# Optimization experiments

Hardware: AMD Instinct MI355X
Metric: run time of the kernel (lower is better)

The kernel has to match this reference:

```python
import jax, jax.numpy as jnp
import numpy as np

T, N, E = 512, 64, 1024   # encoder frames, batch, encoder feature dim
H = 320                   # pred_hidden_size
J = 512                   # joint hidden
V = 29                    # vocab incl. blank
BLANK = V - 1
MAX_SYM = 30              # max_symbols_per_step


def setup_inputs() -> dict:
    key = jax.random.key(0)
    ks = jax.random.split(key, 16)
    sH = 1.0 / np.sqrt(H)
    sE = 1.0 / np.sqrt(E)
    sJ = 1.0 / np.sqrt(J)
    b_o = jax.random.normal(ks[14], (V,), jnp.float32) * 0.1
    b_o = b_o.at[BLANK].add(4.0)  # blank-dominant logits -> realistic sparse emissions
    return {
        "f": jax.random.normal(ks[0], (T, N, E), jnp.float32),
        "f_lens": jax.random.randint(ks[1], (N,), T // 2, T + 1).astype(jnp.int32),
        "emb": jax.random.normal(ks[2], (V - 1, H), jnp.float32) * 0.1,
        "wi0": jax.random.normal(ks[3], (4 * H, H), jnp.float32) * sH,
        "wh0": jax.random.normal(ks[4], (4 * H, H), jnp.float32) * sH,
        "bi0": jax.random.normal(ks[5], (4 * H,), jnp.float32) * 0.05,
        "bh0": jax.random.normal(ks[6], (4 * H,), jnp.float32) * 0.05,
        "wi1": jax.random.normal(ks[7], (4 * H, H), jnp.float32) * sH,
        "wh1": jax.random.normal(ks[8], (4 * H, H), jnp.float32) * sH,
        "bi1": jax.random.normal(ks[9], (4 * H,), jnp.float32) * 0.05,
        "bh1": jax.random.normal(ks[10], (4 * H,), jnp.float32) * 0.05,
        "w_f": jax.random.normal(ks[11], (J, E), jnp.float32) * sE,
        "w_g": jax.random.normal(ks[12], (J, H), jnp.float32) * sH,
        "b_j": jax.random.normal(ks[13], (J,), jnp.float32) * 0.05,
        "w_o": jax.random.normal(ks[15], (V, J), jnp.float32) * sJ,
        "b_o": b_o,
    }


def reference(f, f_lens, emb, wi0, wh0, bi0, bh0, wi1, wh1, bi1, bh1,
              w_f, w_g, b_j, w_o, b_o):
    n = f.shape[1]
    rows = jnp.arange(n)

    def cell(x, h, c, wi, wh, bi, bh):
        g = x @ wi.T + h @ wh.T + (bi + bh)
        i, fg, gg, o = jnp.split(g, 4, axis=-1)  # torch LSTM gate order i,f,g,o
        c2 = jax.nn.sigmoid(fg) * c + jax.nn.sigmoid(i) * jnp.tanh(gg)
        return jax.nn.sigmoid(o) * jnp.tanh(c2), c2

    def pred_step(last_sym, h, c):
        # SOS (=-1) embeds to zeros
        x = jnp.where(last_sym[:, None] < 0, 0.0, emb[jnp.clip(last_sym, 0, V - 2)])
        h0, c0 = cell(x, h[0], c[0], wi0, wh0, bi0, bh0)
        h1, c1 = cell(h0, h[1], c[1], wi1, wh1, bi1, bh1)
        return h1, jnp.stack([h0, h1]), jnp.stack([c0, c1])

    def joint(fi, g):
        hj = jax.nn.relu(fi @ w_f.T + g @ w_g.T + b_j)
        return hj @ w_o.T + b_o

    def cond(st):
        return jnp.any(st[0] < f_lens)

    def body(st):
        time_idx, sym_add, res, res_idx, last, h, c = st
        fi = f[jnp.clip(time_idx, 0, T - 1), rows]            # [N,E] per-element frame
        g, h_new, c_new = pred_step(last, h, c)               # one LSTM step
        sym = jnp.argmax(joint(fi, g), axis=1).astype(jnp.int32)
        active = time_idx < f_lens
        emit = active & (sym != BLANK) & (sym_add < MAX_SYM)
        adv = active & ~emit                                   # blank or symbol cap -> advance time
        slot = jnp.where(emit, res_idx + 1, 0)
        res = res.at[rows, slot].set(jnp.where(emit, sym, res[rows, slot]))
        res_idx = res_idx + emit.astype(jnp.int32)
        sym_add = jnp.where(emit, sym_add + 1, jnp.where(adv, 0, sym_add))
        time_idx = time_idx + adv.astype(jnp.int32)
        last = jnp.where(emit, sym, last)
        m = emit[None, :, None]
        return (time_idx, sym_add, res, res_idx, last,
                jnp.where(m, h_new, h), jnp.where(m, c_new, c))

    init = (jnp.zeros((n,), jnp.int32),                        # time_idx
            jnp.zeros((n,), jnp.int32),                        # symbols_added
            jnp.full((n, MAX_SYM * T), -1, jnp.int32),         # res
            jnp.full((n,), -1, jnp.int32),                     # res_idx
            jnp.full((n,), -1, jnp.int32),                     # pred_g (SOS)
            jnp.zeros((2, n, H), jnp.float32),                 # pred h
            jnp.zeros((2, n, H), jnp.float32))                 # pred c
    st = jax.lax.while_loop(cond, body, init)
    res, res_idx = st[2], st[3]
    return res, res_idx + 1
```

## Files before the change

### kernel.cpp

```cpp
#include <hip/hip_runtime.h>
#include <math.h>

#define T_ 512
#define N_ 64
#define E_ 1024
#define H_ 320
#define HS8_ 40
#define J_ 512
#define V_ 29
#define BLANK_ 28
#define MAXSYM_ 30
#define RESW_ (MAXSYM_ * T_)

__device__ float g_Xi0[V_][4 * H_];
__device__ float g_b1s[4 * H_];
__device__ float g_h0x[2][N_][H_];
__device__ float g_h1x[2][N_][H_];
__device__ float g_gpx[2][N_][8][J_];
__device__ unsigned int g_flag[N_];

#define BM_ 128
#define BN_ 128
#define BK_ 16

__global__ __launch_bounds__(256) void fproj_gemm(
    const float* __restrict__ A, const float* __restrict__ B,
    const float* __restrict__ bj, float* __restrict__ C) {
  __shared__ __align__(16) float As[BK_][BM_ + 4];
  __shared__ __align__(16) float Bs[BK_][BN_ + 4];
  const int tid = threadIdx.x;
  const int m0 = blockIdx.x * BM_;
  const int j0 = blockIdx.y * BN_;
  const int tx = tid & 15, ty = tid >> 4;
  const int sm = tid >> 1;
  const int sk = (tid & 1) << 3;

  float acc[8][8];
#pragma unroll
  for (int i = 0; i < 8; ++i)
#pragma unroll
    for (int j = 0; j < 8; ++j) acc[i][j] = 0.f;

  for (int kc = 0; kc < E_; kc += BK_) {
    float4 av0 = *(const float4*)(A + (size_t)(m0 + sm) * E_ + kc + sk);
    float4 av1 = *(const float4*)(A + (size_t)(m0 + sm) * E_ + kc + sk + 4);
    float4 bv0 = *(const float4*)(B + (size_t)(j0 + sm) * E_ + kc + sk);
    float4 bv1 = *(const float4*)(B + (size_t)(j0 + sm) * E_ + kc + sk + 4);
    __syncthreads();
    As[sk + 0][sm] = av0.x; As[sk + 1][sm] = av0.y;
    As[sk + 2][sm] = av0.z; As[sk + 3][sm] = av0.w;
    As[sk + 4][sm] = av1.x; As[sk + 5][sm] = av1.y;
    As[sk + 6][sm] = av1.z; As[sk + 7][sm] = av1.w;
    Bs[sk + 0][sm] = bv0.x; Bs[sk + 1][sm] = bv0.y;
    Bs[sk + 2][sm] = bv0.z; Bs[sk + 3][sm] = bv0.w;
    Bs[sk + 4][sm] = bv1.x; Bs[sk + 5][sm] = bv1.y;
    Bs[sk + 6][sm] = bv1.z; Bs[sk + 7][sm] = bv1.w;
    __syncthreads();
#pragma unroll
    for (int k = 0; k < BK_; ++k) {
      float a_[8], b_[8];
      *(float4*)&a_[0] = *(const float4*)&As[k][ty * 8];
      *(float4*)&a_[4] = *(const float4*)&As[k][ty * 8 + 4];
      *(float4*)&b_[0] = *(const float4*)&Bs[k][tx * 8];
      *(float4*)&b_[4] = *(const float4*)&Bs[k][tx * 8 + 4];
#pragma unroll
      for (int i = 0; i < 8; ++i)
#pragma unroll
        for (int j = 0; j < 8; ++j) acc[i][j] += a_[i] * b_[j];
    }
  }

#pragma unroll
  for (int i = 0; i < 8; ++i) {
    const size_t m = (size_t)(m0 + ty * 8 + i);
#pragma unroll
    for (int j = 0; j < 8; j += 4) {
      float4 v;
      v.x = acc[i][j + 0] + bj[j0 + tx * 8 + j + 0];
      v.y = acc[i][j + 1] + bj[j0 + tx * 8 + j + 1];
      v.z = acc[i][j + 2] + bj[j0 + tx * 8 + j + 2];
      v.w = acc[i][j + 3] + bj[j0 + tx * 8 + j + 3];
      *(float4*)(C + m * J_ + j0 + tx * 8 + j) = v;
    }
  }
}

__global__ void init_kernel(int* __restrict__ res) {
  const int idx = blockIdx.x * blockDim.x + threadIdx.x;
  if (idx < N_) g_flag[idx] = 0u;
  const int stride = gridDim.x * blockDim.x;
  for (size_t i = idx; i < (size_t)N_ * RESW_; i += stride) res[i] = -1;
}

__global__ __launch_bounds__(256) void xi0_kernel(
    const float* __restrict__ emb, const float* __restrict__ wi0,
    const float* __restrict__ bi0, const float* __restrict__ bh0,
    const float* __restrict__ bi1, const float* __restrict__ bh1) {
  __shared__ __align__(16) float xs[H_];
  const int s = blockIdx.x;
  const int tid = threadIdx.x;
  for (int i = tid; i < H_; i += 256)
    xs[i] = (s < V_ - 1) ? emb[(size_t)s * H_ + i] : 0.f;
  __syncthreads();
  for (int o = tid; o < 4 * H_; o += 256) {
    float acc = bi0[o] + bh0[o];
    if (s < V_ - 1) {
      const float* wr = wi0 + (size_t)o * H_;
      for (int k = 0; k < H_; k += 4) {
        float4 x4 = *(const float4*)&xs[k];
        float4 w4 = *(const float4*)&wr[k];
        acc += x4.x * w4.x + x4.y * w4.y + x4.z * w4.z + x4.w * w4.w;
      }
    }
    g_Xi0[s][o] = acc;
    if (s == 0) g_b1s[o] = bi1[o] + bh1[o];
  }
}

__device__ __forceinline__ float sigmoidf_(float x) {
  return 1.f / (1.f + expf(-x));
}

__device__ __forceinline__ void flag_round8(int row, int tid, int& target) {
  target += 8;
  __syncthreads();
  if (tid == 0) {
    __hip_atomic_fetch_add(&g_flag[row], 1u, __ATOMIC_RELEASE,
                           __HIP_MEMORY_SCOPE_AGENT);
    while (__hip_atomic_load(&g_flag[row], __ATOMIC_ACQUIRE,
                             __HIP_MEMORY_SCOPE_AGENT) < (unsigned)target)
      __builtin_amdgcn_s_sleep(2);
  }
  __syncthreads();
}

__device__ void recompute8(
    int s, int row, int k8, int tid, int par, int& target,
    const float* __restrict__ wh0, const float* __restrict__ wi1,
    const float* __restrict__ wh1, const float* __restrict__ w_g,
    float* h0s, float* h1s, float* gates,
    float& c0, float& c1, float2& gp) {
  const int g = tid / HS8_;
  const int il = tid - g * HS8_;
  const int o = g * H_ + k8 * HS8_ + il;

  if (tid < 4 * HS8_) {
    const float* wr = wh0 + (size_t)o * H_;
    float acc = g_Xi0[s][o];
    for (int kk = 0; kk < H_; kk += 4) {
      float4 h4 = *(const float4*)&h0s[kk];
      float4 w4 = *(const float4*)&wr[kk];
      acc += h4.x * w4.x + h4.y * w4.y + h4.z * w4.z + h4.w * w4.w;
    }
    gates[tid] = acc;
  }
  __syncthreads();
  if (tid < HS8_) {
    float ig = sigmoidf_(gates[tid]);
    float fg = sigmoidf_(gates[HS8_ + tid]);
    float gg = tanhf(gates[2 * HS8_ + tid]);
    float og = sigmoidf_(gates[3 * HS8_ + tid]);
    float c2 = fg * c0 + ig * gg;
    c0 = c2;
    float h2 = og * tanhf(c2);
    __hip_atomic_store(&g_h0x[par][row][k8 * HS8_ + tid], h2, __ATOMIC_RELAXED,
                       __HIP_MEMORY_SCOPE_AGENT);
  }
  float acc1 = 0.f;
  if (tid < 4 * HS8_) {
    const float* whr = wh1 + (size_t)o * H_;
    acc1 = g_b1s[o];
    for (int kk = 0; kk < H_; kk += 4) {
      float4 h4 = *(const float4*)&h1s[kk];
      float4 w4 = *(const float4*)&whr[kk];
      acc1 += h4.x * w4.x + h4.y * w4.y + h4.z * w4.z + h4.w * w4.w;
    }
  }
  flag_round8(row, tid, target);
  h0s[tid] = __hip_atomic_load(&g_h0x[par][row][tid], __ATOMIC_RELAXED,
                               __HIP_MEMORY_SCOPE_AGENT);
  if (tid < H_ - 256)
    h0s[256 + tid] = __hip_atomic_load(&g_h0x[par][row][256 + tid],
                                       __ATOMIC_RELAXED, __HIP_MEMORY_SCOPE_AGENT);
  __syncthreads();
  if (tid < 4 * HS8_) {
    const float* wir = wi1 + (size_t)o * H_;
    for (int kk = 0; kk < H_; kk += 4) {
      float4 x4 = *(const float4*)&h0s[kk];
      float4 w4 = *(const float4*)&wir[kk];
      acc1 += x4.x * w4.x + x4.y * w4.y + x4.z * w4.z + x4.w * w4.w;
    }
    gates[tid] = acc1;
  }
  __syncthreads();
  if (tid < HS8_) {
    float ig = sigmoidf_(gates[tid]);
    float fg = sigmoidf_(gates[HS8_ + tid]);
    float gg = tanhf(gates[2 * HS8_ + tid]);
    float og = sigmoidf_(gates[3 * HS8_ + tid]);
    float c2 = fg * c1 + ig * gg;
    c1 = c2;
    float h2 = og * tanhf(c2);
    h1s[k8 * HS8_ + tid] = h2;
    __hip_atomic_store(&g_h1x[par][row][k8 * HS8_ + tid], h2, __ATOMIC_RELAXED,
                       __HIP_MEMORY_SCOPE_AGENT);
  }
  __syncthreads();
  {
    const float* hsl = &h1s[k8 * HS8_];
#pragma unroll
    for (int jj = 0; jj < 2; ++jj) {
      const int j = tid + jj * 256;
      const float* wgr = w_g + (size_t)j * H_ + k8 * HS8_;
      float a = 0.f;
      for (int kk = 0; kk < HS8_; kk += 4) {
        float4 h4 = *(const float4*)&hsl[kk];
        float4 w4 = *(const float4*)&wgr[kk];
        a += h4.x * w4.x + h4.y * w4.y + h4.z * w4.z + h4.w * w4.w;
      }
      __hip_atomic_store(&g_gpx[par][row][k8][j], a, __ATOMIC_RELAXED,
                         __HIP_MEMORY_SCOPE_AGENT);
    }
  }
  flag_round8(row, tid, target);
  {
    float ax = 0.f, ay = 0.f;
#pragma unroll
    for (int kk = 0; kk < 8; ++kk) {
      ax += __hip_atomic_load(&g_gpx[par][row][kk][2 * tid], __ATOMIC_RELAXED,
                              __HIP_MEMORY_SCOPE_AGENT);
      ay += __hip_atomic_load(&g_gpx[par][row][kk][2 * tid + 1], __ATOMIC_RELAXED,
                              __HIP_MEMORY_SCOPE_AGENT);
    }
    gp.x = ax; gp.y = ay;
  }
  h1s[tid] = __hip_atomic_load(&g_h1x[par][row][tid], __ATOMIC_RELAXED,
                               __HIP_MEMORY_SCOPE_AGENT);
  if (tid < H_ - 256)
    h1s[256 + tid] = __hip_atomic_load(&g_h1x[par][row][256 + tid],
                                       __ATOMIC_RELAXED, __HIP_MEMORY_SCOPE_AGENT);
  __syncthreads();
}

__global__ __launch_bounds__(256, 2) void decode8(
    const float* __restrict__ Fproj, const int* __restrict__ f_lens,
    const float* __restrict__ wh0,
    const float* __restrict__ wi1, const float* __restrict__ wh1,
    const float* __restrict__ w_g,
    const float* __restrict__ w_o, const float* __restrict__ b_o,
    int* __restrict__ res, int* __restrict__ nsym) {
  const int bid = blockIdx.x;
  const int k8 = bid & 7;
  const int row = ((bid >> 3) + 8 * k8) & 63;
  const int tid = threadIdx.x;
  const int f_len = f_lens[row];

  __shared__ __align__(16) float h0s[H_], h1s[H_];
  __shared__ __align__(16) float gates[4 * HS8_];
  __shared__ __align__(16) float hjs[J_];
  __shared__ float logits[32];

  const int v = tid >> 3;
  const int lq = tid & 7;
  float4 wo[16];
  float bo = 0.f;
  if (v < V_) {
#pragma unroll
    for (int q = 0; q < 16; ++q)
      wo[q] = *(const float4*)(w_o + (size_t)v * J_ + lq * 4 + 32 * q);
    bo = b_o[v];
  }

  for (int i = tid; i < H_; i += 256) { h0s[i] = 0.f; h1s[i] = 0.f; }
  float c0 = 0.f, c1 = 0.f;
  float2 gp = {0.f, 0.f};
  int target = 0;
  __syncthreads();

  recompute8(BLANK_, row, k8, tid, 0, target, wh0, wi1, wh1, w_g,
             h0s, h1s, gates, c0, c1, gp);
  int ecount = 1;

  int t_loc = 0, sym_add = 0, res_idx = -1;
  float2 fp = *(const float2*)(Fproj + (size_t)row * J_ + 2 * tid);

  while (t_loc < f_len) {
    const int tn = (t_loc + 1 < T_) ? t_loc + 1 : T_ - 1;
    float2 fpn = *(const float2*)(Fproj + ((size_t)tn * N_ + row) * J_ + 2 * tid);

    float hx = fp.x + gp.x, hy = fp.y + gp.y;
    float2 hj2 = {hx > 0.f ? hx : 0.f, hy > 0.f ? hy : 0.f};
    *(float2*)&hjs[2 * tid] = hj2;
    __syncthreads();

    float p = 0.f;
    if (v < V_) {
#pragma unroll
      for (int q = 0; q < 16; ++q) {
        float4 h4 = *(const float4*)&hjs[lq * 4 + 32 * q];
        p += h4.x * wo[q].x + h4.y * wo[q].y + h4.z * wo[q].z + h4.w * wo[q].w;
      }
    }
    p += __shfl_xor(p, 4, 8);
    p += __shfl_xor(p, 2, 8);
    p += __shfl_xor(p, 1, 8);
    if (v < V_ && lq == 0) logits[v] = p + bo;
    __syncthreads();

    float best = logits[0];
    int bi = 0;
#pragma unroll
    for (int vv = 1; vv < V_; ++vv) {
      float lv = logits[vv];
      if (lv > best) { best = lv; bi = vv; }
    }
    const int emit = (bi != BLANK_) && (sym_add < MAXSYM_);

    if (emit) {
      res_idx += 1;
      if (k8 == 0 && tid == 0) res[(size_t)row * RESW_ + res_idx] = bi;
      sym_add += 1;
      recompute8(bi, row, k8, tid, ecount & 1, target, wh0, wi1, wh1, w_g,
                 h0s, h1s, gates, c0, c1, gp);
      ecount += 1;
    } else {
      sym_add = 0;
      t_loc += 1;
      fp = fpn;
    }
  }

  if (k8 == 0 && tid == 0) nsym[row] = res_idx + 1;
}

extern "C" void kernel_launch(void* const* d_in, const int* in_sizes, int n_in,
                              void* d_out, int out_size, void* d_ws, size_t ws_size,
                              hipStream_t stream) {
  const float* f      = (const float*)d_in[0];
  const int*   f_lens = (const int*)d_in[1];
  const float* emb    = (const float*)d_in[2];
  const float* wi0    = (const float*)d_in[3];
  const float* wh0    = (const float*)d_in[4];
  const float* bi0    = (const float*)d_in[5];
  const float* bh0    = (const float*)d_in[6];
  const float* wi1    = (const float*)d_in[7];
  const float* wh1    = (const float*)d_in[8];
  const float* bi1    = (const float*)d_in[9];
  const float* bh1    = (const float*)d_in[10];
  const float* w_f    = (const float*)d_in[11];
  const float* w_g    = (const float*)d_in[12];
  const float* b_j    = (const float*)d_in[13];
  const float* w_o    = (const float*)d_in[14];
  const float* b_o    = (const float*)d_in[15];

  int* out  = (int*)d_out;
  int* res  = out;
  int* nsym = out + (size_t)N_ * RESW_;

  float* Fproj = (float*)d_ws;

  init_kernel<<<1024, 256, 0, stream>>>(res);
  xi0_kernel<<<V_, 256, 0, stream>>>(emb, wi0, bi0, bh0, bi1, bh1);

  dim3 ggrid(T_ * N_ / BM_, J_ / BN_);
  fproj_gemm<<<ggrid, 256, 0, stream>>>(f, w_f, b_j, Fproj);

  decode8<<<N_ * 8, 256, 0, stream>>>(Fproj, f_lens, wh0, wi1, wh1, w_g,
                                      w_o, b_o, res, nsym);
}
```

Measured before the change: 1.996 ms.

## Fuse encoder projection GEMM into decode kernel with per-tile readiness flags

Merges the Fproj GEMM and the greedy decode into one launch. The first 512 blocks run the decoder and the remaining 1024 blocks compute GEMM tiles, each tile bumping a g_done counter for its pair of timesteps. Decoder blocks spin on those counters before reading the next frame's projection, so decoding overlaps with the GEMM instead of waiting for it to finish. It also folds the xi0 precompute into the init kernel and shortens the spin sleep. The scheme relies on all decoder blocks being co-resident with the GEMM blocks (launch bounds of 4 blocks per CU) to avoid deadlock, and GEMM blocks now compete with decoding for CU resources.

```diff
diff --git a/kernel.cpp b/kernel.cpp
--- a/kernel.cpp
+++ b/kernel.cpp
@@ -12,108 +12,51 @@
 #define MAXSYM_ 30
 #define RESW_ (MAXSYM_ * T_)
 
+#define BM_ 128
+#define BN_ 128
+#define BK_ 16
+#define DECB_ 512
+
 __device__ float g_Xi0[V_][4 * H_];
 __device__ float g_b1s[4 * H_];
 __device__ float g_h0x[2][N_][H_];
 __device__ float g_h1x[2][N_][H_];
 __device__ float g_gpx[2][N_][8][J_];
 __device__ unsigned int g_flag[N_];
-
-#define BM_ 128
-#define BN_ 128
-#define BK_ 16
-
-__global__ __launch_bounds__(256) void fproj_gemm(
-    const float* __restrict__ A, const float* __restrict__ B,
-    const float* __restrict__ bj, float* __restrict__ C) {
-  __shared__ __align__(16) float As[BK_][BM_ + 4];
-  __shared__ __align__(16) float Bs[BK_][BN_ + 4];
-  const int tid = threadIdx.x;
-  const int m0 = blockIdx.x * BM_;
-  const int j0 = blockIdx.y * BN_;
-  const int tx = tid & 15, ty = tid >> 4;
-  const int sm = tid >> 1;
-  const int sk = (tid & 1) << 3;
-
-  float acc[8][8];
-#pragma unroll
-  for (int i = 0; i < 8; ++i)
-#pragma unroll
-    for (int j = 0; j < 8; ++j) acc[i][j] = 0.f;
-
-  for (int kc = 0; kc < E_; kc += BK_) {
-    float4 av0 = *(const float4*)(A + (size_t)(m0 + sm) * E_ + kc + sk);
-    float4 av1 = *(const float4*)(A + (size_t)(m0 + sm) * E_ + kc + sk + 4);
-    float4 bv0 = *(const float4*)(B + (size_t)(j0 + sm) * E_ + kc + sk);
-    float4 bv1 = *(const float4*)(B + (size_t)(j0 + sm) * E_ + kc + sk + 4);
-    __syncthreads();
-    As[sk + 0][sm] = av0.x; As[sk + 1][sm] = av0.y;
-    As[sk + 2][sm] = av0.z; As[sk + 3][sm] = av0.w;
-    As[sk + 4][sm] = av1.x; As[sk + 5][sm] = av1.y;
-    As[sk + 6][sm] = av1.z; As[sk + 7][sm] = av1.w;
-    Bs[sk + 0][sm] = bv0.x; Bs[sk + 1][sm] = bv0.y;
-    Bs[sk + 2][sm] = bv0.z; Bs[sk + 3][sm] = bv0.w;
-    Bs[sk + 4][sm] = bv1.x; Bs[sk + 5][sm] = bv1.y;
-    Bs[sk + 6][sm] = bv1.z; Bs[sk + 7][sm] = bv1.w;
-    __syncthreads();
-#pragma unroll
-    for (int k = 0; k < BK_; ++k) {
-      float a_[8], b_[8];
-      *(float4*)&a_[0] = *(const float4*)&As[k][ty * 8];
-      *(float4*)&a_[4] = *(const float4*)&As[k][ty * 8 + 4];
-      *(float4*)&b_[0] = *(const float4*)&Bs[k][tx * 8];
-      *(float4*)&b_[4] = *(const float4*)&Bs[k][tx * 8 + 4];
-#pragma unroll
-      for (int i = 0; i < 8; ++i)
-#pragma unroll
-        for (int j = 0; j < 8; ++j) acc[i][j] += a_[i] * b_[j];
-    }
-  }
-
-#pragma unroll
-  for (int i = 0; i < 8; ++i) {
-    const size_t m = (size_t)(m0 + ty * 8 + i);
-#pragma unroll
-    for (int j = 0; j < 8; j += 4) {
-      float4 v;
-      v.x = acc[i][j + 0] + bj[j0 + tx * 8 + j + 0];
-      v.y = acc[i][j + 1] + bj[j0 + tx * 8 + j + 1];
-      v.z = acc[i][j + 2] + bj[j0 + tx * 8 + j + 2];
-      v.w = acc[i][j + 3] + bj[j0 + tx * 8 + j + 3];
-      *(float4*)(C + m * J_ + j0 + tx * 8 + j) = v;
-    }
-  }
-}
-
-__global__ void init_kernel(int* __restrict__ res) {
-  const int idx = blockIdx.x * blockDim.x + threadIdx.x;
-  if (idx < N_) g_flag[idx] = 0u;
-  const int stride = gridDim.x * blockDim.x;
-  for (size_t i = idx; i < (size_t)N_ * RESW_; i += stride) res[i] = -1;
-}
-
-__global__ __launch_bounds__(256) void xi0_kernel(
+__device__ unsigned int g_done[T_ / 2];
+
+__global__ __launch_bounds__(256) void init_kernel(
+    int* __restrict__ res,
     const float* __restrict__ emb, const float* __restrict__ wi0,
     const float* __restrict__ bi0, const float* __restrict__ bh0,
     const float* __restrict__ bi1, const float* __restrict__ bh1) {
-  __shared__ __align__(16) float xs[H_];
-  const int s = blockIdx.x;
-  const int tid = threadIdx.x;
-  for (int i = tid; i < H_; i += 256)
-    xs[i] = (s < V_ - 1) ? emb[(size_t)s * H_ + i] : 0.f;
-  __syncthreads();
-  for (int o = tid; o < 4 * H_; o += 256) {
-    float acc = bi0[o] + bh0[o];
-    if (s < V_ - 1) {
-      const float* wr = wi0 + (size_t)o * H_;
-      for (int k = 0; k < H_; k += 4) {
-        float4 x4 = *(const float4*)&xs[k];
-        float4 w4 = *(const float4*)&wr[k];
-        acc += x4.x * w4.x + x4.y * w4.y + x4.z * w4.z + x4.w * w4.w;
-      }
-    }
-    g_Xi0[s][o] = acc;
-    if (s == 0) g_b1s[o] = bi1[o] + bh1[o];
+  const int bid = blockIdx.x, tid = threadIdx.x;
+  if (bid < V_) {
+    __shared__ __align__(16) float xs[H_];
+    for (int i = tid; i < H_; i += 256)
+      xs[i] = (bid < V_ - 1) ? emb[(size_t)bid * H_ + i] : 0.f;
+    __syncthreads();
+    for (int o = tid; o < 4 * H_; o += 256) {
+      float acc = bi0[o] + bh0[o];
+      if (bid < V_ - 1) {
+        const float* wr = wi0 + (size_t)o * H_;
+        for (int k = 0; k < H_; k += 4) {
+          float4 x4 = *(const float4*)&xs[k];
+          float4 w4 = *(const float4*)&wr[k];
+          acc += x4.x * w4.x + x4.y * w4.y + x4.z * w4.z + x4.w * w4.w;
+        }
+      }
+      g_Xi0[bid][o] = acc;
+      if (bid == 0) g_b1s[o] = bi1[o] + bh1[o];
+    }
+  } else {
+    if (bid == V_) {
+      if (tid < N_) g_flag[tid] = 0u;
+      g_done[tid] = 0u;
+    }
+    const size_t i0 = (size_t)(bid - V_) * 256 + tid;
+    const size_t stride = (size_t)(gridDim.x - V_) * 256;
+    for (size_t i = i0; i < (size_t)N_ * RESW_; i += stride) res[i] = -1;
   }
 }
 
@@ -129,7 +72,7 @@
                            __HIP_MEMORY_SCOPE_AGENT);
     while (__hip_atomic_load(&g_flag[row], __ATOMIC_ACQUIRE,
                              __HIP_MEMORY_SCOPE_AGENT) < (unsigned)target)
-      __builtin_amdgcn_s_sleep(2);
+      __builtin_amdgcn_s_sleep(1);
   }
   __syncthreads();
 }
@@ -242,23 +185,98 @@
   __syncthreads();
 }
 
-__global__ __launch_bounds__(256, 2) void decode8(
-    const float* __restrict__ Fproj, const int* __restrict__ f_lens,
+#define GEMM_SMEM_FLOATS (2 * BK_ * (BM_ + 4))
+
+__global__ __launch_bounds__(256, 4) void fused_kernel(
+    const float* __restrict__ f, const float* __restrict__ w_f,
+    const float* __restrict__ b_j,
+    const int* __restrict__ f_lens,
     const float* __restrict__ wh0,
     const float* __restrict__ wi1, const float* __restrict__ wh1,
     const float* __restrict__ w_g,
     const float* __restrict__ w_o, const float* __restrict__ b_o,
-    int* __restrict__ res, int* __restrict__ nsym) {
+    int* __restrict__ res, int* __restrict__ nsym,
+    float* __restrict__ Fproj) {
+  __shared__ __align__(16) float smem[GEMM_SMEM_FLOATS];
   const int bid = blockIdx.x;
+  const int tid = threadIdx.x;
+
+  if (bid >= DECB_) {
+    float* As = smem;
+    float* Bs = smem + BK_ * (BM_ + 4);
+    const int gb = bid - DECB_;
+    const int mt = gb >> 2;
+    const int jq = gb & 3;
+    const int m0 = mt * BM_;
+    const int j0 = jq * BN_;
+    const int tx = tid & 15, ty = tid >> 4;
+    const int sm = tid >> 1;
+    const int sk = (tid & 1) << 3;
+
+    float acc[8][8];
+#pragma unroll
+    for (int i = 0; i < 8; ++i)
+#pragma unroll
+      for (int j = 0; j < 8; ++j) acc[i][j] = 0.f;
+
+    for (int kc = 0; kc < E_; kc += BK_) {
+      float4 av0 = *(const float4*)(f + (size_t)(m0 + sm) * E_ + kc + sk);
+      float4 av1 = *(const float4*)(f + (size_t)(m0 + sm) * E_ + kc + sk + 4);
+      float4 bv0 = *(const float4*)(w_f + (size_t)(j0 + sm) * E_ + kc + sk);
+      float4 bv1 = *(const float4*)(w_f + (size_t)(j0 + sm) * E_ + kc + sk + 4);
+      __syncthreads();
+      As[(sk + 0) * (BM_ + 4) + sm] = av0.x; As[(sk + 1) * (BM_ + 4) + sm] = av0.y;
+      As[(sk + 2) * (BM_ + 4) + sm] = av0.z; As[(sk + 3) * (BM_ + 4) + sm] = av0.w;
+      As[(sk + 4) * (BM_ + 4) + sm] = av1.x; As[(sk + 5) * (BM_ + 4) + sm] = av1.y;
+      As[(sk + 6) * (BM_ + 4) + sm] = av1.z; As[(sk + 7) * (BM_ + 4) + sm] = av1.w;
+      Bs[(sk + 0) * (BN_ + 4) + sm] = bv0.x; Bs[(sk + 1) * (BN_ + 4) + sm] = bv0.y;
+      Bs[(sk + 2) * (BN_ + 4) + sm] = bv0.z; Bs[(sk + 3) * (BN_ + 4) + sm] = bv0.w;
+      Bs[(sk + 4) * (BN_ + 4) + sm] = bv1.x; Bs[(sk + 5) * (BN_ + 4) + sm] = bv1.y;
+      Bs[(sk + 6) * (BN_ + 4) + sm] = bv1.z; Bs[(sk + 7) * (BN_ + 4) + sm] = bv1.w;
+      __syncthreads();
+#pragma unroll
+      for (int k = 0; k < BK_; ++k) {
+        float a_[8], b_[8];
+        *(float4*)&a_[0] = *(const float4*)&As[k * (BM_ + 4) + ty * 8];
+        *(float4*)&a_[4] = *(const float4*)&As[k * (BM_ + 4) + ty * 8 + 4];
+        *(float4*)&b_[0] = *(const float4*)&Bs[k * (BN_ + 4) + tx * 8];
+        *(float4*)&b_[4] = *(const float4*)&Bs[k * (BN_ + 4) + tx * 8 + 4];
+#pragma unroll
+        for (int i = 0; i < 8; ++i)
+#pragma unroll
+          for (int j = 0; j < 8; ++j) acc[i][j] += a_[i] * b_[j];
+      }
+    }
+
+#pragma unroll
+    for (int i = 0; i < 8; ++i) {
+      const size_t m = (size_t)(m0 + ty * 8 + i);
+#pragma unroll
+      for (int j = 0; j < 8; j += 4) {
+        float4 v;
+        v.x = acc[i][j + 0] + b_j[j0 + tx * 8 + j + 0];
+        v.y = acc[i][j + 1] + b_j[j0 + tx * 8 + j + 1];
+        v.z = acc[i][j + 2] + b_j[j0 + tx * 8 + j + 2];
+        v.w = acc[i][j + 3] + b_j[j0 + tx * 8 + j + 3];
+        *(float4*)(Fproj + m * J_ + j0 + tx * 8 + j) = v;
+      }
+    }
+    __syncthreads();
+    if (tid == 0)
+      __hip_atomic_fetch_add(&g_done[mt], 1u, __ATOMIC_RELEASE,
+                             __HIP_MEMORY_SCOPE_AGENT);
+    return;
+  }
+
+  float* h0s    = smem;
+  float* h1s    = h0s + H_;
+  float* gates  = h1s + H_;
+  float* hjs    = gates + 4 * HS8_;
+  float* logits = hjs + J_;
+
   const int k8 = bid & 7;
   const int row = ((bid >> 3) + 8 * k8) & 63;
-  const int tid = threadIdx.x;
   const int f_len = f_lens[row];
-
-  __shared__ __align__(16) float h0s[H_], h1s[H_];
-  __shared__ __align__(16) float gates[4 * HS8_];
-  __shared__ __align__(16) float hjs[J_];
-  __shared__ float logits[32];
 
   const int v = tid >> 3;
   const int lq = tid & 7;
@@ -281,17 +299,32 @@
              h0s, h1s, gates, c0, c1, gp);
   int ecount = 1;
 
+  if (tid == 0) {
+    while (__hip_atomic_load(&g_done[0], __ATOMIC_ACQUIRE,
+                             __HIP_MEMORY_SCOPE_AGENT) < 4u)
+      __builtin_amdgcn_s_sleep(2);
+  }
+  __syncthreads();
+  float2 fp = *(const float2*)(Fproj + (size_t)row * J_ + 2 * tid);
+  int rdy = 0;
+
   int t_loc = 0, sym_add = 0, res_idx = -1;
-  float2 fp = *(const float2*)(Fproj + (size_t)row * J_ + 2 * tid);
 
   while (t_loc < f_len) {
     const int tn = (t_loc + 1 < T_) ? t_loc + 1 : T_ - 1;
-    float2 fpn = *(const float2*)(Fproj + ((size_t)tn * N_ + row) * J_ + 2 * tid);
+    const int tpn = tn >> 1;
+    if (tid == 0 && rdy < tpn) {
+      while (__hip_atomic_load(&g_done[tpn], __ATOMIC_ACQUIRE,
+                               __HIP_MEMORY_SCOPE_AGENT) < 4u)
+        __builtin_amdgcn_s_sleep(2);
+    }
 
     float hx = fp.x + gp.x, hy = fp.y + gp.y;
     float2 hj2 = {hx > 0.f ? hx : 0.f, hy > 0.f ? hy : 0.f};
     *(float2*)&hjs[2 * tid] = hj2;
     __syncthreads();
+    if (rdy < tpn) rdy = tpn;
+    float2 fpn = *(const float2*)(Fproj + ((size_t)tn * N_ + row) * J_ + 2 * tid);
 
     float p = 0.f;
     if (v < V_) {
@@ -359,12 +392,8 @@
 
   float* Fproj = (float*)d_ws;
 
-  init_kernel<<<1024, 256, 0, stream>>>(res);
-  xi0_kernel<<<V_, 256, 0, stream>>>(emb, wi0, bi0, bh0, bi1, bh1);
-
-  dim3 ggrid(T_ * N_ / BM_, J_ / BN_);
-  fproj_gemm<<<ggrid, 256, 0, stream>>>(f, w_f, b_j, Fproj);
-
-  decode8<<<N_ * 8, 256, 0, stream>>>(Fproj, f_lens, wh0, wi1, wh1, w_g,
-                                      w_o, b_o, res, nsym);
-}
+  init_kernel<<<1024, 256, 0, stream>>>(res, emb, wi0, bi0, bh0, bi1, bh1);
+
+  fused_kernel<<<DECB_ + 1024, 256, 0, stream>>>(
+      f, w_f, b_j, f_lens, wh0, wi1, wh1, w_g, w_o, b_o, res, nsym, Fproj);
+}
```

After: 2.994 ms. 50.1% more time.

## Fuse init, embedding-gate precompute and projection GEMM into one launch

Applied to the files above, without the earlier changes.

Merges the result-buffer init, the Xi0 embedding-gate precompute and the encoder projection GEMM into a single kernel. Extra blocks beyond the GEMM grid do the precompute and a vectorized int4 fill. It also pads the B shared tile to avoid LDS bank conflicts and shortens the spin-wait sleep in the decode barrier. This saves two kernel launches and their serialization, but adds divergent block roles and more polling traffic in the decode loop.

```diff
diff --git a/kernel.cpp b/kernel.cpp
--- a/kernel.cpp
+++ b/kernel.cpp
@@ -12,6 +12,11 @@
 #define MAXSYM_ 30
 #define RESW_ (MAXSYM_ * T_)
 
+#define BM_ 128
+#define BN_ 128
+#define BK_ 16
+#define GEMMB_ 1024
+
 __device__ float g_Xi0[V_][4 * H_];
 __device__ float g_b1s[4 * H_];
 __device__ float g_h0x[2][N_][H_];
@@ -19,21 +24,60 @@
 __device__ float g_gpx[2][N_][8][J_];
 __device__ unsigned int g_flag[N_];
 
-#define BM_ 128
-#define BN_ 128
-#define BK_ 16
-
-__global__ __launch_bounds__(256) void fproj_gemm(
+#define BSW_ 144
+__device__ __forceinline__ int padcol(int c) { return c + ((c >> 5) << 2); }
+
+__global__ __launch_bounds__(256) void gemm_init_kernel(
     const float* __restrict__ A, const float* __restrict__ B,
-    const float* __restrict__ bj, float* __restrict__ C) {
+    const float* __restrict__ bj, float* __restrict__ C,
+    const float* __restrict__ emb, const float* __restrict__ wi0,
+    const float* __restrict__ bi0, const float* __restrict__ bh0,
+    const float* __restrict__ bi1, const float* __restrict__ bh1,
+    int* __restrict__ res) {
+  const int bid = blockIdx.x;
+  const int tid = threadIdx.x;
+
+  if (bid >= GEMMB_) {
+    const int ab = bid - GEMMB_;
+    if (ab < V_) {
+      __shared__ __align__(16) float xs[H_];
+      for (int i = tid; i < H_; i += 256)
+        xs[i] = (ab < V_ - 1) ? emb[(size_t)ab * H_ + i] : 0.f;
+      __syncthreads();
+      for (int o = tid; o < 4 * H_; o += 256) {
+        float acc = bi0[o] + bh0[o];
+        if (ab < V_ - 1) {
+          const float* wr = wi0 + (size_t)o * H_;
+          for (int k = 0; k < H_; k += 4) {
+            float4 x4 = *(const float4*)&xs[k];
+            float4 w4 = *(const float4*)&wr[k];
+            acc += x4.x * w4.x + x4.y * w4.y + x4.z * w4.z + x4.w * w4.w;
+          }
+        }
+        g_Xi0[ab][o] = acc;
+        if (ab == 0) g_b1s[o] = bi1[o] + bh1[o];
+      }
+    } else {
+      if (ab == V_ && tid < N_) g_flag[tid] = 0u;
+      const int fb = ab - V_;
+      int4* r4 = (int4*)res;
+      const size_t tot = (size_t)N_ * RESW_ / 4;
+      const size_t i0 = (size_t)fb * 256 + tid;
+      const int4 mval = {-1, -1, -1, -1};
+      for (size_t i = i0; i < tot; i += 3 * 256) r4[i] = mval;
+    }
+    return;
+  }
+
   __shared__ __align__(16) float As[BK_][BM_ + 4];
-  __shared__ __align__(16) float Bs[BK_][BN_ + 4];
-  const int tid = threadIdx.x;
-  const int m0 = blockIdx.x * BM_;
-  const int j0 = blockIdx.y * BN_;
+  __shared__ __align__(16) float Bs[BK_][BSW_];
+  const int m0 = blockIdx.x / 4 * BM_;
+  const int j0 = (blockIdx.x & 3) * BN_;
   const int tx = tid & 15, ty = tid >> 4;
   const int sm = tid >> 1;
   const int sk = (tid & 1) << 3;
+  const int smP = padcol(sm);
+  const int bcol = padcol(tx * 8);
 
   float acc[8][8];
 #pragma unroll
@@ -51,18 +95,18 @@
     As[sk + 2][sm] = av0.z; As[sk + 3][sm] = av0.w;
     As[sk + 4][sm] = av1.x; As[sk + 5][sm] = av1.y;
     As[sk + 6][sm] = av1.z; As[sk + 7][sm] = av1.w;
-    Bs[sk + 0][sm] = bv0.x; Bs[sk + 1][sm] = bv0.y;
-    Bs[sk + 2][sm] = bv0.z; Bs[sk + 3][sm] = bv0.w;
-    Bs[sk + 4][sm] = bv1.x; Bs[sk + 5][sm] = bv1.y;
-    Bs[sk + 6][sm] = bv1.z; Bs[sk + 7][sm] = bv1.w;
+    Bs[sk + 0][smP] = bv0.x; Bs[sk + 1][smP] = bv0.y;
+    Bs[sk + 2][smP] = bv0.z; Bs[sk + 3][smP] = bv0.w;
+    Bs[sk + 4][smP] = bv1.x; Bs[sk + 5][smP] = bv1.y;
+    Bs[sk + 6][smP] = bv1.z; Bs[sk + 7][smP] = bv1.w;
     __syncthreads();
 #pragma unroll
     for (int k = 0; k < BK_; ++k) {
       float a_[8], b_[8];
       *(float4*)&a_[0] = *(const float4*)&As[k][ty * 8];
       *(float4*)&a_[4] = *(const float4*)&As[k][ty * 8 + 4];
-      *(float4*)&b_[0] = *(const float4*)&Bs[k][tx * 8];
-      *(float4*)&b_[4] = *(const float4*)&Bs[k][tx * 8 + 4];
+      *(float4*)&b_[0] = *(const float4*)&Bs[k][bcol];
+      *(float4*)&b_[4] = *(const float4*)&Bs[k][bcol + 4];
 #pragma unroll
       for (int i = 0; i < 8; ++i)
 #pragma unroll
@@ -85,38 +129,6 @@
   }
 }
 
-__global__ void init_kernel(int* __restrict__ res) {
-  const int idx = blockIdx.x * blockDim.x + threadIdx.x;
-  if (idx < N_) g_flag[idx] = 0u;
-  const int stride = gridDim.x * blockDim.x;
-  for (size_t i = idx; i < (size_t)N_ * RESW_; i += stride) res[i] = -1;
-}
-
-__global__ __launch_bounds__(256) void xi0_kernel(
-    const float* __restrict__ emb, const float* __restrict__ wi0,
-    const float* __restrict__ bi0, const float* __restrict__ bh0,
-    const float* __restrict__ bi1, const float* __restrict__ bh1) {
-  __shared__ __align__(16) float xs[H_];
-  const int s = blockIdx.x;
-  const int tid = threadIdx.x;
-  for (int i = tid; i < H_; i += 256)
-    xs[i] = (s < V_ - 1) ? emb[(size_t)s * H_ + i] : 0.f;
-  __syncthreads();
-  for (int o = tid; o < 4 * H_; o += 256) {
-    float acc = bi0[o] + bh0[o];
-    if (s < V_ - 1) {
-      const float* wr = wi0 + (size_t)o * H_;
-      for (int k = 0; k < H_; k += 4) {
-        float4 x4 = *(const float4*)&xs[k];
-        float4 w4 = *(const float4*)&wr[k];
-        acc += x4.x * w4.x + x4.y * w4.y + x4.z * w4.z + x4.w * w4.w;
-      }
-    }
-    g_Xi0[s][o] = acc;
-    if (s == 0) g_b1s[o] = bi1[o] + bh1[o];
-  }
-}
-
 __device__ __forceinline__ float sigmoidf_(float x) {
   return 1.f / (1.f + expf(-x));
 }
@@ -129,7 +141,7 @@
                            __HIP_MEMORY_SCOPE_AGENT);
     while (__hip_atomic_load(&g_flag[row], __ATOMIC_ACQUIRE,
                              __HIP_MEMORY_SCOPE_AGENT) < (unsigned)target)
-      __builtin_amdgcn_s_sleep(2);
+      __builtin_amdgcn_s_sleep(1);
   }
   __syncthreads();
 }
@@ -359,11 +371,8 @@
 
   float* Fproj = (float*)d_ws;
 
-  init_kernel<<<1024, 256, 0, stream>>>(res);
-  xi0_kernel<<<V_, 256, 0, stream>>>(emb, wi0, bi0, bh0, bi1, bh1);
-
-  dim3 ggrid(T_ * N_ / BM_, J_ / BN_);
-  fproj_gemm<<<ggrid, 256, 0, stream>>>(f, w_f, b_j, Fproj);
+  gemm_init_kernel<<<GEMMB_ + 32, 256, 0, stream>>>(
+      f, w_f, b_j, Fproj, emb, wi0, bi0, bh0, bi1, bh1, res);
 
   decode8<<<N_ * 8, 256, 0, stream>>>(Fproj, f_lens, wh0, wi1, wh1, w_g,
                                       w_o, b_o, res, nsym);
```

New measurement: 1.932 ms. 3.2% less time.
